# Kernel tuning notes

Hardware: AMD Instinct MI355X
Metric: run time of the kernel (lower is better)

The kernel has to match this reference:

```python
import jax, jax.numpy as jnp
import numpy as np

TOP_K = 8
ROUTE_SCALE = 2.5
NUM_EXPERTS = 64


def setup_inputs() -> dict:
    key = jax.random.key(0)
    k1, k2, k3 = jax.random.split(key, 3)
    x = jax.random.normal(k1, (16384, 4096), dtype=jnp.float32)
    gate_weight = jax.random.normal(k2, (NUM_EXPERTS, 4096), dtype=jnp.float32) * 0.02
    expert_bias = jax.random.normal(k3, (NUM_EXPERTS,), dtype=jnp.float32) * 0.01
    return {"x": x, "gate_weight": gate_weight, "expert_bias": expert_bias}


def reference(x, gate_weight, expert_bias):
    # gate linear: [T, dim] @ [dim, E] -> [T, E]
    logits = jnp.einsum("td,ed->te", x, gate_weight)
    scores = jax.nn.sigmoid(logits.astype(jnp.float32))  # score_func == 'sigmoid'
    # expert_bias branch: top-k over biased scores, gather unbiased scores
    _, selected_experts_indices = jax.lax.top_k(scores + expert_bias[None, :], TOP_K)
    top_scores = jnp.take_along_axis(scores, selected_experts_indices, axis=1)
    # route_norm (sigmoid normalization)
    denom = top_scores.sum(axis=-1, keepdims=True) + 1e-20
    top_scores = top_scores / denom * ROUTE_SCALE
    # histogram over selected expert indices (torch.histc returns float)
    flat_idx = selected_experts_indices.reshape(-1)
    num_tokens_per_expert = jnp.zeros((NUM_EXPERTS,), jnp.float32).at[flat_idx].add(1.0)
    return top_scores, selected_experts_indices, num_tokens_per_expert
```

## Files before the change

kernel.cpp:

```cpp
#include <hip/hip_runtime.h>
#include <math.h>

#define NTOK 16384
#define DIM  4096
#define NE   64
#define TOPK 8
#define SPLITK 8
#define NSPW (DIM / 32 / SPLITK)
#define ROUTE_SCALE 2.5f

typedef __attribute__((ext_vector_type(8))) short short8v;
typedef __attribute__((ext_vector_type(4))) float f32x4;

__device__ __forceinline__ void split3_pack(const float* v, uint4& b0, uint4& b1, uint4& b2)
{
    uint p0[8], p1[8], p2[8];
#pragma unroll
    for (int j = 0; j < 8; ++j) {
        const float xv = v[j];
        const uint  u0 = __float_as_uint(xv) & 0xffff0000u;
        const float f0 = __uint_as_float(u0);
        const float r  = xv - f0;
        const uint  u1 = __float_as_uint(r) & 0xffff0000u;
        const float f1 = __uint_as_float(u1);
        const float r2 = r - f1;
        const uint  u2 = __float_as_uint(r2) & 0xffff0000u;
        p0[j] = u0; p1[j] = u1; p2[j] = u2;
    }
    b0 = make_uint4(p0[1] | (p0[0] >> 16), p0[3] | (p0[2] >> 16),
                    p0[5] | (p0[4] >> 16), p0[7] | (p0[6] >> 16));
    b1 = make_uint4(p1[1] | (p1[0] >> 16), p1[3] | (p1[2] >> 16),
                    p1[5] | (p1[4] >> 16), p1[7] | (p1[6] >> 16));
    b2 = make_uint4(p2[1] | (p2[0] >> 16), p2[3] | (p2[2] >> 16),
                    p2[5] | (p2[4] >> 16), p2[7] | (p2[6] >> 16));
}

__global__ __launch_bounds__(256)
void prep_w(const float* __restrict__ gw, uint4* __restrict__ wS)
{
    const int tid  = blockIdx.x * 256 + threadIdx.x;
    const int lane = tid & 63;
    const int nt   = (tid >> 6) & 3;
    const int ks   = tid >> 8;
    const int e    = nt * 16 + (lane & 15);
    const int kb   = ks * 32 + (lane >> 4) * 8;
    float v[8];
    *(float4*)&v[0] = *(const float4*)&gw[(size_t)e * DIM + kb];
    *(float4*)&v[4] = *(const float4*)&gw[(size_t)e * DIM + kb + 4];
    uint4 b0, b1, b2;
    split3_pack(v, b0, b1, b2);
    const size_t base = (size_t)(ks * 4 + nt) * 3 * 64 + lane;
    wS[base] = b0; wS[base + 64] = b1; wS[base + 128] = b2;
}

#define MFMA6(A0, A1, A2, B0, B1, B2, ACC) do {                              \
    ACC = __builtin_amdgcn_mfma_f32_16x16x32_bf16(A2, B0, ACC, 0, 0, 0);     \
    ACC = __builtin_amdgcn_mfma_f32_16x16x32_bf16(A1, B1, ACC, 0, 0, 0);     \
    ACC = __builtin_amdgcn_mfma_f32_16x16x32_bf16(A0, B2, ACC, 0, 0, 0);     \
    ACC = __builtin_amdgcn_mfma_f32_16x16x32_bf16(A1, B0, ACC, 0, 0, 0);     \
    ACC = __builtin_amdgcn_mfma_f32_16x16x32_bf16(A0, B1, ACC, 0, 0, 0);     \
    ACC = __builtin_amdgcn_mfma_f32_16x16x32_bf16(A0, B0, ACC, 0, 0, 0);     \
} while (0)

__global__ __launch_bounds__(512, 4)
void router_fused(const float* __restrict__ x, const uint4* __restrict__ wS,
                  const float* __restrict__ bias, float* __restrict__ out)
{
    __shared__ float part_lds[SPLITK][32][NE];
    __shared__ int   hist[NE];

    const int t    = threadIdx.x;
    const int lane = t & 63;
    const int wv   = __builtin_amdgcn_readfirstlane(t >> 6);
    const int r15  = lane & 15;
    const int g    = lane >> 4;
    const int tok0 = blockIdx.x * 32;

    if (t < NE) hist[t] = 0;

    const float* xr0 = x + (size_t)(tok0 + r15) * DIM + g * 8;
    const float* xr1 = x + (size_t)(tok0 + 16 + r15) * DIM + g * 8;
    const uint4* wq  = wS + lane;

    f32x4 acc[4][2];
#pragma unroll
    for (int nt = 0; nt < 4; ++nt) {
        acc[nt][0] = (f32x4){0.f, 0.f, 0.f, 0.f};
        acc[nt][1] = (f32x4){0.f, 0.f, 0.f, 0.f};
    }

    const int s0 = wv * NSPW;
#pragma unroll 1
    for (int s = s0; s < s0 + NSPW; ++s) {
        float a8[8];
        uint4 u0, u1, u2;
        *(float4*)&a8[0] = *(const float4*)(xr0 + (size_t)s * 32);
        *(float4*)&a8[4] = *(const float4*)(xr0 + (size_t)s * 32 + 4);
        split3_pack(a8, u0, u1, u2);
        const short8v A0h0 = *(short8v*)&u0, A1h0 = *(short8v*)&u1, A2h0 = *(short8v*)&u2;
        *(float4*)&a8[0] = *(const float4*)(xr1 + (size_t)s * 32);
        *(float4*)&a8[4] = *(const float4*)(xr1 + (size_t)s * 32 + 4);
        split3_pack(a8, u0, u1, u2);
        const short8v A0h1 = *(short8v*)&u0, A1h1 = *(short8v*)&u1, A2h1 = *(short8v*)&u2;
        const size_t sb = (size_t)s * 768;
#pragma unroll
        for (int nt = 0; nt < 4; ++nt) {
            const uint4 b0 = wq[sb + nt * 192];
            const uint4 b1 = wq[sb + nt * 192 + 64];
            const uint4 b2 = wq[sb + nt * 192 + 128];
            MFMA6(A0h0, A1h0, A2h0, *(const short8v*)&b0, *(const short8v*)&b1,
                  *(const short8v*)&b2, acc[nt][0]);
            MFMA6(A0h1, A1h1, A2h1, *(const short8v*)&b0, *(const short8v*)&b1,
                  *(const short8v*)&b2, acc[nt][1]);
        }
    }

#pragma unroll
    for (int nt = 0; nt < 4; ++nt)
#pragma unroll
        for (int G = 0; G < 2; ++G)
#pragma unroll
            for (int q = 0; q < 4; ++q)
                part_lds[wv][G * 16 + g * 4 + q][nt * 16 + r15] = acc[nt][G][q];

    __syncthreads();

    const float bias_l = bias[lane];
#pragma unroll 1
    for (int i = 0; i < 4; ++i) {
        const int tok = wv * 4 + i;
        float logit = 0.f;
#pragma unroll
        for (int kh = 0; kh < SPLITK; ++kh)
            logit += part_lds[kh][tok][lane];
        const float s = 1.f / (1.f + expf(-logit));
        float myv  = s + bias_l;
        float outv = 0.f;
        int   outi = 0;
        float sum  = 0.f;
#pragma unroll
        for (int k = 0; k < TOPK; ++k) {
            float cv = myv;
            int   ci = lane;
#pragma unroll
            for (int off = 32; off; off >>= 1) {
                float ov = __shfl_xor(cv, off, 64);
                int   oi = __shfl_xor(ci, off, 64);
                if (ov > cv || (ov == cv && oi < ci)) { cv = ov; ci = oi; }
            }
            float ts = __shfl(s, ci, 64);
            sum += ts;
            if (lane == k)  { outv = ts; outi = ci; }
            if (lane == ci) { myv = -1e30f; }
        }
        const float denom = sum + 1e-20f;
        const size_t gt = (size_t)tok0 + tok;
        if (lane < TOPK) {
            out[gt * TOPK + lane] = (outv / denom) * ROUTE_SCALE;
            out[(size_t)NTOK * TOPK + gt * TOPK + lane] = (float)outi;
            atomicAdd(&hist[outi], 1);
        }
    }

    __syncthreads();
    if (t < NE) {
        int cgt = hist[t];
        if (cgt) atomicAdd(&out[(size_t)NTOK * TOPK * 2 + t], (float)cgt);
    }
}

extern "C" void kernel_launch(void* const* d_in, const int* in_sizes, int n_in,
                              void* d_out, int out_size, void* d_ws, size_t ws_size,
                              hipStream_t stream)
{
    const float* x    = (const float*)d_in[0];
    const float* gw   = (const float*)d_in[1];
    const float* bias = (const float*)d_in[2];
    float* out = (float*)d_out;
    uint4* wS  = (uint4*)d_ws;

    hipMemsetAsync(out + (size_t)NTOK * TOPK * 2, 0, NE * sizeof(float), stream);

    prep_w<<<128, 256, 0, stream>>>(gw, wS);
    router_fused<<<NTOK / 32, 512, 0, stream>>>(x, wS, bias, out);
}
```

Baseline: 99.81 us.

## Stream x tiles into double-buffered LDS via async global_load_lds and prefetch weights

Each wave's x slice no longer comes straight from global memory into registers. It is now copied asynchronously into a per-wave, double-buffered, XOR-swizzled LDS region with global_load_lds. The split-bf16 weight fragments for the next k-step are prefetched into registers while the MFMAs of the current step run. Explicit vmcnt waits and sched barriers order the pipeline. The goal is to hide global-memory latency on this bandwidth-bound GEMM, at the cost of extra LDS reads, more VGPRs for the B registers, and hand-tuned wait counts that could break if the instruction order changes.

```diff
diff --git a/kernel.cpp b/kernel.cpp
--- a/kernel.cpp
+++ b/kernel.cpp
@@ -6,7 +6,7 @@
 #define NE   64
 #define TOPK 8
 #define SPLITK 8
-#define NSPW (DIM / 32 / SPLITK)
+#define NSPW 16
 #define ROUTE_SCALE 2.5f
 
 typedef __attribute__((ext_vector_type(8))) short short8v;
@@ -53,6 +53,14 @@
     wS[base] = b0; wS[base + 64] = b1; wS[base + 128] = b2;
 }
 
+__device__ __forceinline__ void gld_lds16(const float* g, float* l)
+{
+    __builtin_amdgcn_global_load_lds(
+        (const __attribute__((address_space(1))) unsigned int*)g,
+        (__attribute__((address_space(3))) unsigned int*)l,
+        16, 0, 0);
+}
+
 #define MFMA6(A0, A1, A2, B0, B1, B2, ACC) do {                              \
     ACC = __builtin_amdgcn_mfma_f32_16x16x32_bf16(A2, B0, ACC, 0, 0, 0);     \
     ACC = __builtin_amdgcn_mfma_f32_16x16x32_bf16(A1, B1, ACC, 0, 0, 0);     \
@@ -62,11 +70,14 @@
     ACC = __builtin_amdgcn_mfma_f32_16x16x32_bf16(A0, B0, ACC, 0, 0, 0);     \
 } while (0)
 
+#define SB __builtin_amdgcn_sched_barrier(0)
+#define WAITV(N) do { SB; asm volatile("s_waitcnt vmcnt(" #N ")" ::: "memory"); SB; } while (0)
+
 __global__ __launch_bounds__(512, 4)
 void router_fused(const float* __restrict__ x, const uint4* __restrict__ wS,
                   const float* __restrict__ bias, float* __restrict__ out)
 {
-    __shared__ float part_lds[SPLITK][32][NE];
+    __shared__ float pool[SPLITK * 2 * 1024];
     __shared__ int   hist[NE];
 
     const int t    = threadIdx.x;
@@ -75,12 +86,18 @@
     const int r15  = lane & 15;
     const int g    = lane >> 4;
     const int tok0 = blockIdx.x * 32;
+    const int ks0  = wv * NSPW;
 
     if (t < NE) hist[t] = 0;
 
-    const float* xr0 = x + (size_t)(tok0 + r15) * DIM + g * 8;
-    const float* xr1 = x + (size_t)(tok0 + 16 + r15) * DIM + g * 8;
-    const uint4* wq  = wS + lane;
+    const int lr  = lane >> 3;
+    const int swz = (lane & 7) ^ lr;
+    const float* gsrc0 = x + (size_t)(tok0 +  0 + lr) * DIM + ks0 * 32 + swz * 4;
+    const float* gsrc1 = x + (size_t)(tok0 +  8 + lr) * DIM + ks0 * 32 + swz * 4;
+    const float* gsrc2 = x + (size_t)(tok0 + 16 + lr) * DIM + ks0 * 32 + swz * 4;
+    const float* gsrc3 = x + (size_t)(tok0 + 24 + lr) * DIM + ks0 * 32 + swz * 4;
+
+    const uint4* wq = wS + lane;
 
     f32x4 acc[4][2];
 #pragma unroll
@@ -88,40 +105,74 @@
         acc[nt][0] = (f32x4){0.f, 0.f, 0.f, 0.f};
         acc[nt][1] = (f32x4){0.f, 0.f, 0.f, 0.f};
     }
-
-    const int s0 = wv * NSPW;
+    uint4 B[12];
+
+    const int jr = r15 >> 3;
+    const int R  = r15 & 7;
+    const int q0 = (2 * g) ^ R;
+    const int q1 = (2 * g + 1) ^ R;
+
+#define DMAC(c) do {                                                         \
+        float* ldst = &pool[(size_t)(wv * 2 + ((c) & 1)) * 1024];            \
+        gld_lds16(gsrc0 + (size_t)(c) * 32, ldst);                           \
+        gld_lds16(gsrc1 + (size_t)(c) * 32, ldst + 256);                     \
+        gld_lds16(gsrc2 + (size_t)(c) * 32, ldst + 512);                     \
+        gld_lds16(gsrc3 + (size_t)(c) * 32, ldst + 768);                     \
+    } while (0)
+#define LOADB(cg) do {                                                       \
+        const size_t sgb = (size_t)(ks0 + (cg)) * 768;                       \
+        _Pragma("unroll")                                                    \
+        for (int nt = 0; nt < 4; ++nt)                                       \
+            _Pragma("unroll")                                                \
+            for (int sp = 0; sp < 3; ++sp)                                   \
+                B[nt * 3 + sp] = wq[sgb + nt * 192 + sp * 64];               \
+    } while (0)
+
+    LOADB(0);
+    DMAC(0);
+    DMAC(1);
+
 #pragma unroll 1
-    for (int s = s0; s < s0 + NSPW; ++s) {
-        float a8[8];
-        uint4 u0, u1, u2;
-        *(float4*)&a8[0] = *(const float4*)(xr0 + (size_t)s * 32);
-        *(float4*)&a8[4] = *(const float4*)(xr0 + (size_t)s * 32 + 4);
-        split3_pack(a8, u0, u1, u2);
-        const short8v A0h0 = *(short8v*)&u0, A1h0 = *(short8v*)&u1, A2h0 = *(short8v*)&u2;
-        *(float4*)&a8[0] = *(const float4*)(xr1 + (size_t)s * 32);
-        *(float4*)&a8[4] = *(const float4*)(xr1 + (size_t)s * 32 + 4);
-        split3_pack(a8, u0, u1, u2);
-        const short8v A0h1 = *(short8v*)&u0, A1h1 = *(short8v*)&u1, A2h1 = *(short8v*)&u2;
-        const size_t sb = (size_t)s * 768;
-#pragma unroll
-        for (int nt = 0; nt < 4; ++nt) {
-            const uint4 b0 = wq[sb + nt * 192];
-            const uint4 b1 = wq[sb + nt * 192 + 64];
-            const uint4 b2 = wq[sb + nt * 192 + 128];
-            MFMA6(A0h0, A1h0, A2h0, *(const short8v*)&b0, *(const short8v*)&b1,
-                  *(const short8v*)&b2, acc[nt][0]);
-            MFMA6(A0h1, A1h1, A2h1, *(const short8v*)&b0, *(const short8v*)&b1,
-                  *(const short8v*)&b2, acc[nt][1]);
+    for (int c = 0; c < NSPW; ++c) {
+        if (c == NSPW - 1) { WAITV(0); } else { WAITV(4); }
+        {
+            const float* sbase = &pool[(size_t)(wv * 2 + (c & 1)) * 1024];
+            float a8[8]; uint4 u0, u1, u2;
+            *(float4*)&a8[0] = *(const float4*)&sbase[jr * 256 + R * 32 + q0 * 4];
+            *(float4*)&a8[4] = *(const float4*)&sbase[jr * 256 + R * 32 + q1 * 4];
+            split3_pack(a8, u0, u1, u2);
+            const short8v A0h0 = *(short8v*)&u0, A1h0 = *(short8v*)&u1, A2h0 = *(short8v*)&u2;
+            *(float4*)&a8[0] = *(const float4*)&sbase[(jr + 2) * 256 + R * 32 + q0 * 4];
+            *(float4*)&a8[4] = *(const float4*)&sbase[(jr + 2) * 256 + R * 32 + q1 * 4];
+            split3_pack(a8, u0, u1, u2);
+            const short8v A0h1 = *(short8v*)&u0, A1h1 = *(short8v*)&u1, A2h1 = *(short8v*)&u2;
+#pragma unroll
+            for (int nt = 0; nt < 4; ++nt) {
+                MFMA6(A0h0, A1h0, A2h0, *(const short8v*)&B[nt * 3 + 0],
+                      *(const short8v*)&B[nt * 3 + 1], *(const short8v*)&B[nt * 3 + 2],
+                      acc[nt][0]);
+                MFMA6(A0h1, A1h1, A2h1, *(const short8v*)&B[nt * 3 + 0],
+                      *(const short8v*)&B[nt * 3 + 1], *(const short8v*)&B[nt * 3 + 2],
+                      acc[nt][1]);
+            }
         }
-    }
-
+        SB;
+        if (c + 1 < NSPW) LOADB(c + 1);
+        SB;
+        if (c + 2 < NSPW) DMAC(c + 2);
+        SB;
+    }
+#undef DMAC
+#undef LOADB
+
+    float (*part)[32][NE] = (float (*)[32][NE])pool;
 #pragma unroll
     for (int nt = 0; nt < 4; ++nt)
 #pragma unroll
         for (int G = 0; G < 2; ++G)
 #pragma unroll
             for (int q = 0; q < 4; ++q)
-                part_lds[wv][G * 16 + g * 4 + q][nt * 16 + r15] = acc[nt][G][q];
+                part[wv][G * 16 + g * 4 + q][nt * 16 + r15] = acc[nt][G][q];
 
     __syncthreads();
 
@@ -132,7 +183,7 @@
         float logit = 0.f;
 #pragma unroll
         for (int kh = 0; kh < SPLITK; ++kh)
-            logit += part_lds[kh][tok][lane];
+            logit += part[kh][tok][lane];
         const float s = 1.f / (1.f + expf(-logit));
         float myv  = s + bias_l;
         float outv = 0.f;
```

After: 97.44 us. 2.4% less time.
